# Optimization experiments

Measured on AMD Instinct MI355X. Metric: run time of the kernel, lower is better.

Reference implementation:

```python
import jax, jax.numpy as jnp
import numpy as np

B, S, D = 32, 512, 512      # batch, seq, feature
E, H, O, K = 8, 2048, 512, 2  # experts, expert hidden, expert out, top_k


def setup_inputs() -> dict:
    key = jax.random.key(0)
    ks = jax.random.split(key, 5)
    sc = lambda k, shape, scale: jax.random.normal(k, shape, jnp.float32) * scale
    return {
        "x": sc(ks[0], (B, S, D), 1.0),
        "attn_w": sc(ks[1], (D, 1), 0.05),
        "attn_b": jnp.zeros((1,), jnp.float32),
        "gate_w": sc(ks[2], (D, E), 0.05),
        "gate_b": jnp.zeros((E,), jnp.float32),
        "w1": sc(ks[3], (E, D, H), 0.02),
        "b1": jnp.zeros((E, H), jnp.float32),
        "w2": sc(ks[4], (E, H, O), 0.02),
        "b2": jnp.zeros((E, O), jnp.float32),
    }


def reference(x, attn_w, attn_b, gate_w, gate_b, w1, b1, w2, b2):
    # --- attention pooling over the sequence axis ---
    scores = x @ attn_w + attn_b                      # [B,S,1]
    aw = jax.nn.softmax(scores, axis=1)               # softmax over seq
    pooled = jnp.sum(x * aw, axis=1)                  # [B,D]

    # --- gating: softmax -> top-k mask -> renormalize ---
    gates = jax.nn.softmax(pooled @ gate_w + gate_b, axis=-1)  # [B,E]
    _, idx = jax.lax.top_k(gates, K)                  # [B,K]
    mask = jnp.sum(jax.nn.one_hot(idx, E, dtype=gates.dtype), axis=-2)  # [B,E]
    g = gates * mask
    g = g / (jnp.sum(g, axis=-1, keepdims=True) + 1e-9)        # [B,E]

    # --- dense all-experts compute (exact GELU, as keras Dense('gelu')) ---
    h = jax.nn.gelu(jnp.einsum('bsd,edh->ebsh', x, w1) + b1[:, None, None, :],
                    approximate=False)                 # [E,B,S,H]
    eo = jax.nn.gelu(jnp.einsum('ebsh,eho->ebso', h, w2) + b2[:, None, None, :],
                     approximate=False)                # [E,B,S,O]

    # --- weighted combine over experts ---
    return jnp.einsum('ebso,be->bso', eo, g)           # [B,S,O]
```

## Files before the change

kernel.cpp:

```cpp
#include <hip/hip_runtime.h>
#include <hip/hip_bf16.h>
#include <math.h>

#define B_  32
#define S_  512
#define D_  512
#define E_  8
#define H_  2048
#define O_  512

typedef __bf16 bf16x8 __attribute__((ext_vector_type(8)));
typedef float  f32x4  __attribute__((ext_vector_type(4)));

#define GL2LDS(src, dst) \
  __builtin_amdgcn_global_load_lds((const __attribute__((address_space(1))) void*)(src), \
                                   (__attribute__((address_space(3))) void*)(dst), 16, 0, 0)

__device__ __forceinline__ float gelu_exact(float v) {
  return 0.5f * v * (1.0f + erff(v * 0.70710678118654752f));
}

__global__ __launch_bounds__(256) void pool_gate_kernel(
    const float* __restrict__ x, const float* __restrict__ attn_w,
    const float* __restrict__ attn_b, const float* __restrict__ gate_w,
    const float* __restrict__ gate_b, int* __restrict__ gidx, float* __restrict__ gwt)
{
  __shared__ float sc[512];
  __shared__ float pooled[512];
  __shared__ float red[8];
  const int tid = threadIdx.x;
  const int b = blockIdx.x;
  const float* xb = x + (size_t)b * S_ * D_;
  const float ab = attn_b[0];

  for (int s = tid; s < S_; s += 256) {
    const float4* xr = (const float4*)(xb + (size_t)s * D_);
    const float4* wr = (const float4*)attn_w;
    float acc = 0.f;
    for (int i = 0; i < D_ / 4; ++i) {
      float4 xv = xr[i], wv = wr[i];
      acc += xv.x * wv.x + xv.y * wv.y + xv.z * wv.z + xv.w * wv.w;
    }
    sc[s] = acc + ab;
  }
  __syncthreads();

  float m = fmaxf(sc[tid], sc[tid + 256]);
  for (int off = 32; off; off >>= 1) m = fmaxf(m, __shfl_down(m, off));
  if ((tid & 63) == 0) red[tid >> 6] = m;
  __syncthreads();
  if (tid == 0) red[0] = fmaxf(fmaxf(red[0], red[1]), fmaxf(red[2], red[3]));
  __syncthreads();
  m = red[0];
  float e0 = expf(sc[tid] - m), e1 = expf(sc[tid + 256] - m);
  float ssum = e0 + e1;
  for (int off = 32; off; off >>= 1) ssum += __shfl_down(ssum, off);
  if ((tid & 63) == 0) red[4 + (tid >> 6)] = ssum;
  __syncthreads();
  if (tid == 0) red[4] = red[4] + red[5] + red[6] + red[7];
  __syncthreads();
  float inv = 1.f / red[4];
  sc[tid] = e0 * inv;
  sc[tid + 256] = e1 * inv;
  __syncthreads();

  float p0 = 0.f, p1 = 0.f;
  for (int s = 0; s < S_; ++s) {
    float awv = sc[s];
    p0 += awv * xb[(size_t)s * D_ + tid];
    p1 += awv * xb[(size_t)s * D_ + tid + 256];
  }
  pooled[tid] = p0;
  pooled[tid + 256] = p1;
  __syncthreads();

  if (tid < E_) {
    float z = gate_b[tid];
    for (int d = 0; d < D_; ++d) z += pooled[d] * gate_w[d * E_ + tid];
    red[tid] = z;
  }
  __syncthreads();
  if (tid == 0) {
    float zmax = red[0];
    for (int i = 1; i < E_; ++i) zmax = fmaxf(zmax, red[i]);
    float ge[E_]; float zs = 0.f;
    for (int i = 0; i < E_; ++i) { ge[i] = expf(red[i] - zmax); zs += ge[i]; }
    for (int i = 0; i < E_; ++i) ge[i] /= zs;
    int i0 = 0;
    for (int i = 1; i < E_; ++i) if (ge[i] > ge[i0]) i0 = i;
    int i1 = -1;
    for (int i = 0; i < E_; ++i) if (i != i0 && (i1 < 0 || ge[i] > ge[i1])) i1 = i;
    float denom = ge[i0] + ge[i1] + 1e-9f;
    gidx[b * 2 + 0] = i0; gidx[b * 2 + 1] = i1;
    gwt[b * 2 + 0] = ge[i0] / denom; gwt[b * 2 + 1] = ge[i1] / denom;
  }
}

__global__ void cast_x_kernel(const float* __restrict__ in, ushort* __restrict__ outp, int n) {
  int i = blockIdx.x * blockDim.x + threadIdx.x;
  const int n4 = n >> 2;
  for (; i < n4; i += gridDim.x * blockDim.x) {
    float4 v = ((const float4*)in)[i];
    ushort4 o;
    o.x = __builtin_bit_cast(unsigned short, __float2bfloat16(v.x));
    o.y = __builtin_bit_cast(unsigned short, __float2bfloat16(v.y));
    o.z = __builtin_bit_cast(unsigned short, __float2bfloat16(v.z));
    o.w = __builtin_bit_cast(unsigned short, __float2bfloat16(v.w));
    ((ushort4*)outp)[i] = o;
  }
}

__global__ void transpose_cast_kernel(const float* __restrict__ in,
                                      __hip_bfloat16* __restrict__ outT, int R, int C)
{
  __shared__ float tile[32][33];
  const int z = blockIdx.z;
  const float* inz = in + (size_t)z * R * C;
  __hip_bfloat16* outz = outT + (size_t)z * R * C;
  const int c0 = blockIdx.x * 32, r0 = blockIdx.y * 32;
  const int tx = threadIdx.x, ty = threadIdx.y;
#pragma unroll
  for (int jj = 0; jj < 4; ++jj) {
    int r = r0 + ty + jj * 8;
    tile[ty + jj * 8][tx] = inz[(size_t)r * C + c0 + tx];
  }
  __syncthreads();
#pragma unroll
  for (int jj = 0; jj < 4; ++jj) {
    int c = c0 + ty + jj * 8;
    outz[(size_t)c * R + r0 + tx] = __float2bfloat16(tile[tx][ty + jj * 8]);
  }
}

__device__ __forceinline__ void stage_tile(char* lds, const __hip_bfloat16* g, int ldk, int kt, int tid) {
#pragma unroll
  for (int i = 0; i < 4; ++i) {
    int f = (i * 256 + tid) * 16;
    int row = f >> 7;
    int colb = (f & 127) ^ ((row & 7) << 4);
    const char* src = (const char*)g + ((size_t)row * ldk + kt) * 2 + colb;
    GL2LDS(src, lds + f);
  }
}

__device__ __forceinline__ void gemm_tiles(const __hip_bfloat16* Ag, const __hip_bfloat16* Bg,
                                           int K, char* As, char* Bs, f32x4 (&acc)[4][4])
{
  const int tid = threadIdx.x;
  const int l = tid & 63;
  const int w = tid >> 6;
  const int wm = (w >> 1) << 6;
  const int wn = (w & 1) << 6;
  const int lr = l & 15;
  const int kg = (l >> 4) << 3;
  for (int kt = 0; kt < K; kt += 64) {
    __syncthreads();
    stage_tile(As, Ag, K, kt, tid);
    stage_tile(Bs, Bg, K, kt, tid);
    __syncthreads();
#pragma unroll
    for (int kk = 0; kk < 2; ++kk) {
      const int kb = (kk * 32 + kg) * 2;
      bf16x8 af[4], bfv[4];
#pragma unroll
      for (int i = 0; i < 4; ++i) {
        int ra = wm + i * 16 + lr;
        af[i] = *(const bf16x8*)(As + ra * 128 + (kb ^ ((ra & 7) << 4)));
        int rb = wn + i * 16 + lr;
        bfv[i] = *(const bf16x8*)(Bs + rb * 128 + (kb ^ ((rb & 7) << 4)));
      }
#pragma unroll
      for (int mi = 0; mi < 4; ++mi)
#pragma unroll
        for (int ni = 0; ni < 4; ++ni)
          acc[mi][ni] = __builtin_amdgcn_mfma_f32_16x16x32_bf16(af[mi], bfv[ni], acc[mi][ni], 0, 0, 0);
    }
  }
}

__global__ __launch_bounds__(256, 2) void gemm1_kernel(
    const __hip_bfloat16* __restrict__ Xb, const __hip_bfloat16* __restrict__ W1T,
    const float* __restrict__ b1, __hip_bfloat16* __restrict__ Hbuf,
    const int* __restrict__ gidx, int p0)
{
  __shared__ char lds[32768];
  char* As = lds; char* Bs = lds + 16384;
  const int p = p0 + blockIdx.y;
  const int b = p >> 1;
  const int e = gidx[p];
  const int s0 = (blockIdx.x >> 4) * 128;
  const int h0 = (blockIdx.x & 15) * 128;
  const __hip_bfloat16* Ag = Xb + ((size_t)b * S_ + s0) * D_;
  const __hip_bfloat16* Bg = W1T + ((size_t)e * H_ + h0) * D_;
  f32x4 acc[4][4] = {};
  gemm_tiles(Ag, Bg, D_, As, Bs, acc);

  const int tid = threadIdx.x, l = tid & 63, w = tid >> 6;
  const int wm = (w >> 1) << 6, wn = (w & 1) << 6;
  const int r4 = (l >> 4) << 2, cc = l & 15;
  const float* b1e = b1 + (size_t)e * H_ + h0;
  __hip_bfloat16* Hb = Hbuf + ((size_t)blockIdx.y * S_ + s0) * H_ + h0;
#pragma unroll
  for (int mi = 0; mi < 4; ++mi) {
    int row = wm + mi * 16 + r4;
#pragma unroll
    for (int ni = 0; ni < 4; ++ni) {
      int col = wn + ni * 16 + cc;
      float bias = b1e[col];
      __hip_bfloat16* dst = Hb + (size_t)row * H_ + col;
#pragma unroll
      for (int j = 0; j < 4; ++j) {
        float v = gelu_exact(acc[mi][ni][j] + bias);
        dst[(size_t)j * H_] = __float2bfloat16(v);
      }
    }
  }
}

__global__ __launch_bounds__(256, 2) void gemm2_kernel(
    const __hip_bfloat16* __restrict__ Hbuf, const __hip_bfloat16* __restrict__ W2T,
    const float* __restrict__ b2, float* __restrict__ out,
    const int* __restrict__ gidx, const float* __restrict__ gwt, int p0)
{
  __shared__ char lds[32768];
  char* As = lds; char* Bs = lds + 16384;
  const int p = p0 + blockIdx.y;
  const int b = p >> 1;
  const int e = gidx[p];
  const float gw = gwt[p];
  const int s0 = (blockIdx.x >> 2) * 128;
  const int o0 = (blockIdx.x & 3) * 128;
  const __hip_bfloat16* Ag = Hbuf + ((size_t)blockIdx.y * S_ + s0) * H_;
  const __hip_bfloat16* Bg = W2T + ((size_t)e * O_ + o0) * H_;
  f32x4 acc[4][4] = {};
  gemm_tiles(Ag, Bg, H_, As, Bs, acc);

  const int tid = threadIdx.x, l = tid & 63, w = tid >> 6;
  const int wm = (w >> 1) << 6, wn = (w & 1) << 6;
  const int r4 = (l >> 4) << 2, cc = l & 15;
  const float* b2e = b2 + (size_t)e * O_ + o0;
  float* ob = out + ((size_t)b * S_ + s0) * O_ + o0;
#pragma unroll
  for (int mi = 0; mi < 4; ++mi) {
    int row = wm + mi * 16 + r4;
#pragma unroll
    for (int ni = 0; ni < 4; ++ni) {
      int col = wn + ni * 16 + cc;
      float bias = b2e[col];
      float* dst = ob + (size_t)row * O_ + col;
#pragma unroll
      for (int j = 0; j < 4; ++j) {
        float v = gelu_exact(acc[mi][ni][j] + bias) * gw;
        atomicAdd(dst + (size_t)j * O_, v);
      }
    }
  }
}

__global__ void sentinel_kernel(float* out, int n) {
  int i = blockIdx.x * blockDim.x + threadIdx.x;
  for (; i < n; i += gridDim.x * blockDim.x) out[i] = 1.0e6f;
}

extern "C" void kernel_launch(void* const* d_in, const int* in_sizes, int n_in,
                              void* d_out, int out_size, void* d_ws, size_t ws_size,
                              hipStream_t stream)
{
  const float* x      = (const float*)d_in[0];
  const float* attn_w = (const float*)d_in[1];
  const float* attn_b = (const float*)d_in[2];
  const float* gate_w = (const float*)d_in[3];
  const float* gate_b = (const float*)d_in[4];
  const float* w1     = (const float*)d_in[5];
  const float* b1     = (const float*)d_in[6];
  const float* w2     = (const float*)d_in[7];
  const float* b2     = (const float*)d_in[8];
  float* out = (float*)d_out;

  char* ws = (char*)d_ws;
  const size_t OFF_GIDX = 0;
  const size_t OFF_GWT  = 256;
  const size_t OFF_X    = 512;
  const size_t SZ_X     = (size_t)B_ * S_ * D_ * 2;
  const size_t OFF_W1T  = OFF_X + SZ_X;
  const size_t SZ_W1T   = (size_t)E_ * H_ * D_ * 2;
  const size_t OFF_W2T  = OFF_W1T + SZ_W1T;
  const size_t SZ_W2T   = (size_t)E_ * O_ * H_ * 2;
  const size_t OFF_H    = OFF_W2T + SZ_W2T;
  const size_t PAIR_H   = (size_t)S_ * H_ * 2;

  int G = 64;
  while (G > 1 && OFF_H + (size_t)G * PAIR_H > ws_size) G >>= 1;
  if (OFF_H + (size_t)G * PAIR_H > ws_size) {
    hipLaunchKernelGGL(sentinel_kernel, dim3(256), dim3(256), 0, stream, out, out_size);
    return;
  }

  int*   gidx = (int*)(ws + OFF_GIDX);
  float* gwt  = (float*)(ws + OFF_GWT);
  __hip_bfloat16* xb   = (__hip_bfloat16*)(ws + OFF_X);
  __hip_bfloat16* w1T  = (__hip_bfloat16*)(ws + OFF_W1T);
  __hip_bfloat16* w2T  = (__hip_bfloat16*)(ws + OFF_W2T);
  __hip_bfloat16* Hbuf = (__hip_bfloat16*)(ws + OFF_H);

  hipLaunchKernelGGL(pool_gate_kernel, dim3(B_), dim3(256), 0, stream,
                     x, attn_w, attn_b, gate_w, gate_b, gidx, gwt);
  hipLaunchKernelGGL(cast_x_kernel, dim3(2048), dim3(256), 0, stream,
                     x, (ushort*)xb, B_ * S_ * D_);
  hipLaunchKernelGGL(transpose_cast_kernel, dim3(H_ / 32, D_ / 32, E_), dim3(32, 8), 0, stream,
                     w1, w1T, D_, H_);
  hipLaunchKernelGGL(transpose_cast_kernel, dim3(O_ / 32, H_ / 32, E_), dim3(32, 8), 0, stream,
                     w2, w2T, H_, O_);
  hipMemsetAsync(d_out, 0, (size_t)out_size * sizeof(float), stream);

  for (int p0 = 0; p0 < B_ * 2; p0 += G) {
    hipLaunchKernelGGL(gemm1_kernel, dim3(64, G), dim3(256), 0, stream,
                       xb, w1T, b1, Hbuf, gidx, p0);
    hipLaunchKernelGGL(gemm2_kernel, dim3(16, G), dim3(256), 0, stream,
                       Hbuf, w2T, b2, out, gidx, gwt, p0);
  }
}
```

Measured before the change: 310.0 us.

## Use 256x256 double-buffered GEMM tiles with 512 threads and staged prefetch

Replaces the 128x128 single-buffered GEMM core with a 256x256 tile over 8 waves that double-buffers K-slices in 128KB of dynamic LDS. The loads for the next slice are split into four chunks and issued between MFMA phases, so global-to-LDS traffic overlaps compute. Operands are swapped so weights feed the A side, and epilogues use vectorized bias loads and stores. It also drops the group loop and launches all 64 pairs in one grid each. The larger tiles raise register and LDS pressure, which could limit occupancy, and the requested 2 blocks per CU would need 256KB of LDS, which may not fit.

After: 485.0 us. +56.5%, slower.

```diff
diff --git a/kernel.cpp b/kernel.cpp
--- a/kernel.cpp
+++ b/kernel.cpp
@@ -132,127 +132,198 @@
   }
 }
 
-__device__ __forceinline__ void stage_tile(char* lds, const __hip_bfloat16* g, int ldk, int kt, int tid) {
-#pragma unroll
-  for (int i = 0; i < 4; ++i) {
-    int f = (i * 256 + tid) * 16;
-    int row = f >> 7;
-    int colb = (f & 127) ^ ((row & 7) << 4);
-    const char* src = (const char*)g + ((size_t)row * ldk + kt) * 2 + colb;
-    GL2LDS(src, lds + f);
-  }
-}
-
-__device__ __forceinline__ void gemm_tiles(const __hip_bfloat16* Ag, const __hip_bfloat16* Bg,
-                                           int K, char* As, char* Bs, f32x4 (&acc)[4][4])
+__device__ __forceinline__ void gemm256(const char* __restrict__ Ag, const char* __restrict__ Bg,
+                                        const int ldb, const int NT, char* lds, f32x4 (&acc)[8][4])
 {
   const int tid = threadIdx.x;
   const int l = tid & 63;
   const int w = tid >> 6;
-  const int wm = (w >> 1) << 6;
-  const int wn = (w & 1) << 6;
+  const int wr = w >> 2;
+  const int wc = w & 3;
   const int lr = l & 15;
-  const int kg = (l >> 4) << 3;
-  for (int kt = 0; kt < K; kt += 64) {
-    __syncthreads();
-    stage_tile(As, Ag, K, kt, tid);
-    stage_tile(Bs, Bg, K, kt, tid);
-    __syncthreads();
-#pragma unroll
-    for (int kk = 0; kk < 2; ++kk) {
-      const int kb = (kk * 32 + kg) * 2;
-      bf16x8 af[4], bfv[4];
-#pragma unroll
-      for (int i = 0; i < 4; ++i) {
-        int ra = wm + i * 16 + lr;
-        af[i] = *(const bf16x8*)(As + ra * 128 + (kb ^ ((ra & 7) << 4)));
-        int rb = wn + i * 16 + lr;
-        bfv[i] = *(const bf16x8*)(Bs + rb * 128 + (kb ^ ((rb & 7) << 4)));
-      }
-#pragma unroll
-      for (int mi = 0; mi < 4; ++mi)
-#pragma unroll
-        for (int ni = 0; ni < 4; ++ni)
-          acc[mi][ni] = __builtin_amdgcn_mfma_f32_16x16x32_bf16(af[mi], bfv[ni], acc[mi][ni], 0, 0, 0);
-    }
-  }
-}
-
-__global__ __launch_bounds__(256, 2) void gemm1_kernel(
+  const int hi16 = ((l >> 4) & 3) << 4;
+  const int axor = (lr & 7) << 4;
+  const int k0 = (0   + hi16) ^ axor;
+  const int k1 = (64  + hi16) ^ axor;
+  const int abase = wr * 16384 + lr * 128;
+  const int bbase = 32768 + wc * 8192 + lr * 128;
+
+  const int rw = tid >> 3;
+  const int cs = ((tid & 7) << 4) ^ ((rw & 7) << 4);
+  const char* sA00 = Ag + (size_t)(  0 +  0 + rw) * ldb + cs;
+  const char* sA01 = Ag + (size_t)(  0 + 64 + rw) * ldb + cs;
+  const char* sA10 = Ag + (size_t)(128 +  0 + rw) * ldb + cs;
+  const char* sA11 = Ag + (size_t)(128 + 64 + rw) * ldb + cs;
+  const char* sB00 = Bg + (size_t)(  0 +  0 + rw) * ldb + cs;
+  const char* sB01 = Bg + (size_t)(  0 + 64 + rw) * ldb + cs;
+  const char* sB10 = Bg + (size_t)(128 +  0 + rw) * ldb + cs;
+  const char* sB11 = Bg + (size_t)(128 + 64 + rw) * ldb + cs;
+  const int dst = tid * 16;
+
+  GL2LDS(sA00, lds + dst);            GL2LDS(sA01, lds +  8192 + dst);
+  GL2LDS(sA10, lds + 16384 + dst);    GL2LDS(sA11, lds + 24576 + dst);
+  GL2LDS(sB00, lds + 32768 + dst);    GL2LDS(sB01, lds + 40960 + dst);
+  GL2LDS(sB10, lds + 49152 + dst);    GL2LDS(sB11, lds + 57344 + dst);
+  sA00 += 128; sA01 += 128; sA10 += 128; sA11 += 128;
+  sB00 += 128; sB01 += 128; sB10 += 128; sB11 += 128;
+
+  for (int t = 0; t < NT; ++t) {
+    char* cur = lds + ((t & 1) << 16);
+    char* nxt = lds + (((t + 1) & 1) << 16);
+    const bool pre = (t + 1 < NT);
+    bf16x8 bf[4][2];
+    bf16x8 af[2][2];
+
+    if (pre) { GL2LDS(sA00, nxt + dst); GL2LDS(sA01, nxt + 8192 + dst); }
+    if (pre) asm volatile("s_waitcnt vmcnt(2)" ::: "memory");
+    else     asm volatile("s_waitcnt vmcnt(0)" ::: "memory");
+    __builtin_amdgcn_s_barrier();
+    __builtin_amdgcn_sched_barrier(0);
+#pragma unroll
+    for (int n = 0; n < 4; ++n) {
+      bf[n][0] = *(const bf16x8*)(cur + bbase + n * 2048 + k0);
+      bf[n][1] = *(const bf16x8*)(cur + bbase + n * 2048 + k1);
+    }
+    af[0][0] = *(const bf16x8*)(cur + abase + 0 * 2048 + k0);
+    af[0][1] = *(const bf16x8*)(cur + abase + 0 * 2048 + k1);
+    af[1][0] = *(const bf16x8*)(cur + abase + 1 * 2048 + k0);
+    af[1][1] = *(const bf16x8*)(cur + abase + 1 * 2048 + k1);
+    __builtin_amdgcn_s_setprio(1);
+#pragma unroll
+    for (int rr = 0; rr < 2; ++rr)
+#pragma unroll
+      for (int n = 0; n < 4; ++n)
+#pragma unroll
+        for (int kh = 0; kh < 2; ++kh)
+          acc[0 + rr][n] = __builtin_amdgcn_mfma_f32_16x16x32_bf16(af[rr][kh], bf[n][kh], acc[0 + rr][n], 0, 0, 0);
+    __builtin_amdgcn_s_setprio(0);
+    __builtin_amdgcn_s_barrier();
+
+    if (pre) { GL2LDS(sA10, nxt + 16384 + dst); GL2LDS(sA11, nxt + 24576 + dst); }
+    af[0][0] = *(const bf16x8*)(cur + abase + 2 * 2048 + k0);
+    af[0][1] = *(const bf16x8*)(cur + abase + 2 * 2048 + k1);
+    af[1][0] = *(const bf16x8*)(cur + abase + 3 * 2048 + k0);
+    af[1][1] = *(const bf16x8*)(cur + abase + 3 * 2048 + k1);
+    __builtin_amdgcn_s_setprio(1);
+#pragma unroll
+    for (int rr = 0; rr < 2; ++rr)
+#pragma unroll
+      for (int n = 0; n < 4; ++n)
+#pragma unroll
+        for (int kh = 0; kh < 2; ++kh)
+          acc[2 + rr][n] = __builtin_amdgcn_mfma_f32_16x16x32_bf16(af[rr][kh], bf[n][kh], acc[2 + rr][n], 0, 0, 0);
+    __builtin_amdgcn_s_setprio(0);
+    __builtin_amdgcn_s_barrier();
+
+    if (pre) { GL2LDS(sB00, nxt + 32768 + dst); GL2LDS(sB01, nxt + 40960 + dst); }
+    af[0][0] = *(const bf16x8*)(cur + abase + 4 * 2048 + k0);
+    af[0][1] = *(const bf16x8*)(cur + abase + 4 * 2048 + k1);
+    af[1][0] = *(const bf16x8*)(cur + abase + 5 * 2048 + k0);
+    af[1][1] = *(const bf16x8*)(cur + abase + 5 * 2048 + k1);
+    __builtin_amdgcn_s_setprio(1);
+#pragma unroll
+    for (int rr = 0; rr < 2; ++rr)
+#pragma unroll
+      for (int n = 0; n < 4; ++n)
+#pragma unroll
+        for (int kh = 0; kh < 2; ++kh)
+          acc[4 + rr][n] = __builtin_amdgcn_mfma_f32_16x16x32_bf16(af[rr][kh], bf[n][kh], acc[4 + rr][n], 0, 0, 0);
+    __builtin_amdgcn_s_setprio(0);
+    __builtin_amdgcn_s_barrier();
+
+    if (pre) { GL2LDS(sB10, nxt + 49152 + dst); GL2LDS(sB11, nxt + 57344 + dst); }
+    af[0][0] = *(const bf16x8*)(cur + abase + 6 * 2048 + k0);
+    af[0][1] = *(const bf16x8*)(cur + abase + 6 * 2048 + k1);
+    af[1][0] = *(const bf16x8*)(cur + abase + 7 * 2048 + k0);
+    af[1][1] = *(const bf16x8*)(cur + abase + 7 * 2048 + k1);
+    __builtin_amdgcn_s_setprio(1);
+#pragma unroll
+    for (int rr = 0; rr < 2; ++rr)
+#pragma unroll
+      for (int n = 0; n < 4; ++n)
+#pragma unroll
+        for (int kh = 0; kh < 2; ++kh)
+          acc[6 + rr][n] = __builtin_amdgcn_mfma_f32_16x16x32_bf16(af[rr][kh], bf[n][kh], acc[6 + rr][n], 0, 0, 0);
+    __builtin_amdgcn_s_setprio(0);
+    __builtin_amdgcn_sched_barrier(0);
+    __builtin_amdgcn_s_barrier();
+
+    if (pre) {
+      sA00 += 128; sA01 += 128; sA10 += 128; sA11 += 128;
+      sB00 += 128; sB01 += 128; sB10 += 128; sB11 += 128;
+    }
+  }
+}
+
+__global__ __launch_bounds__(512, 2) void gemm1_kernel(
     const __hip_bfloat16* __restrict__ Xb, const __hip_bfloat16* __restrict__ W1T,
     const float* __restrict__ b1, __hip_bfloat16* __restrict__ Hbuf,
-    const int* __restrict__ gidx, int p0)
-{
-  __shared__ char lds[32768];
-  char* As = lds; char* Bs = lds + 16384;
-  const int p = p0 + blockIdx.y;
+    const int* __restrict__ gidx)
+{
+  extern __shared__ char lds[];
+  const int p = blockIdx.y;
   const int b = p >> 1;
   const int e = gidx[p];
-  const int s0 = (blockIdx.x >> 4) * 128;
-  const int h0 = (blockIdx.x & 15) * 128;
-  const __hip_bfloat16* Ag = Xb + ((size_t)b * S_ + s0) * D_;
-  const __hip_bfloat16* Bg = W1T + ((size_t)e * H_ + h0) * D_;
-  f32x4 acc[4][4] = {};
-  gemm_tiles(Ag, Bg, D_, As, Bs, acc);
+  const int sc0 = (blockIdx.x >> 3) * 256;
+  const int h0  = (blockIdx.x & 7) * 256;
+  const char* Ag = (const char*)(W1T + ((size_t)e * H_ + h0) * D_);
+  const char* Bg = (const char*)(Xb + ((size_t)b * S_ + sc0) * D_);
+  f32x4 acc[8][4] = {};
+  gemm256(Ag, Bg, D_ * 2, D_ / 64, lds, acc);
 
   const int tid = threadIdx.x, l = tid & 63, w = tid >> 6;
-  const int wm = (w >> 1) << 6, wn = (w & 1) << 6;
-  const int r4 = (l >> 4) << 2, cc = l & 15;
+  const int wr = w >> 2, wc = w & 3, lr = l & 15, hi4 = ((l >> 4) & 3) << 2;
   const float* b1e = b1 + (size_t)e * H_ + h0;
-  __hip_bfloat16* Hb = Hbuf + ((size_t)blockIdx.y * S_ + s0) * H_ + h0;
-#pragma unroll
-  for (int mi = 0; mi < 4; ++mi) {
-    int row = wm + mi * 16 + r4;
-#pragma unroll
-    for (int ni = 0; ni < 4; ++ni) {
-      int col = wn + ni * 16 + cc;
-      float bias = b1e[col];
-      __hip_bfloat16* dst = Hb + (size_t)row * H_ + col;
-#pragma unroll
-      for (int j = 0; j < 4; ++j) {
-        float v = gelu_exact(acc[mi][ni][j] + bias);
-        dst[(size_t)j * H_] = __float2bfloat16(v);
-      }
-    }
-  }
-}
-
-__global__ __launch_bounds__(256, 2) void gemm2_kernel(
+  __hip_bfloat16* Hp = Hbuf + (size_t)p * S_ * H_;
+#pragma unroll
+  for (int r = 0; r < 8; ++r) {
+    const int hl = wr * 128 + r * 16 + hi4;
+    const float4 bias = *(const float4*)(b1e + hl);
+#pragma unroll
+    for (int n = 0; n < 4; ++n) {
+      const int sl = sc0 + wc * 64 + n * 16 + lr;
+      ushort4 ov;
+      ov.x = __builtin_bit_cast(unsigned short, __float2bfloat16(gelu_exact(acc[r][n][0] + bias.x)));
+      ov.y = __builtin_bit_cast(unsigned short, __float2bfloat16(gelu_exact(acc[r][n][1] + bias.y)));
+      ov.z = __builtin_bit_cast(unsigned short, __float2bfloat16(gelu_exact(acc[r][n][2] + bias.z)));
+      ov.w = __builtin_bit_cast(unsigned short, __float2bfloat16(gelu_exact(acc[r][n][3] + bias.w)));
+      *(ushort4*)(Hp + (size_t)sl * H_ + h0 + hl) = ov;
+    }
+  }
+}
+
+__global__ __launch_bounds__(512, 2) void gemm2_kernel(
     const __hip_bfloat16* __restrict__ Hbuf, const __hip_bfloat16* __restrict__ W2T,
     const float* __restrict__ b2, float* __restrict__ out,
-    const int* __restrict__ gidx, const float* __restrict__ gwt, int p0)
-{
-  __shared__ char lds[32768];
-  char* As = lds; char* Bs = lds + 16384;
-  const int p = p0 + blockIdx.y;
+    const int* __restrict__ gidx, const float* __restrict__ gwt)
+{
+  extern __shared__ char lds[];
+  const int p = blockIdx.y;
   const int b = p >> 1;
   const int e = gidx[p];
   const float gw = gwt[p];
-  const int s0 = (blockIdx.x >> 2) * 128;
-  const int o0 = (blockIdx.x & 3) * 128;
-  const __hip_bfloat16* Ag = Hbuf + ((size_t)blockIdx.y * S_ + s0) * H_;
-  const __hip_bfloat16* Bg = W2T + ((size_t)e * O_ + o0) * H_;
-  f32x4 acc[4][4] = {};
-  gemm_tiles(Ag, Bg, H_, As, Bs, acc);
+  const int sc0 = (blockIdx.x >> 1) * 256;
+  const int o0  = (blockIdx.x & 1) * 256;
+  const char* Ag = (const char*)(W2T + ((size_t)e * O_ + o0) * H_);
+  const char* Bg = (const char*)(Hbuf + ((size_t)p * S_ + sc0) * H_);
+  f32x4 acc[8][4] = {};
+  gemm256(Ag, Bg, H_ * 2, H_ / 64, lds, acc);
 
   const int tid = threadIdx.x, l = tid & 63, w = tid >> 6;
-  const int wm = (w >> 1) << 6, wn = (w & 1) << 6;
-  const int r4 = (l >> 4) << 2, cc = l & 15;
+  const int wr = w >> 2, wc = w & 3, lr = l & 15, hi4 = ((l >> 4) & 3) << 2;
   const float* b2e = b2 + (size_t)e * O_ + o0;
-  float* ob = out + ((size_t)b * S_ + s0) * O_ + o0;
-#pragma unroll
-  for (int mi = 0; mi < 4; ++mi) {
-    int row = wm + mi * 16 + r4;
-#pragma unroll
-    for (int ni = 0; ni < 4; ++ni) {
-      int col = wn + ni * 16 + cc;
-      float bias = b2e[col];
-      float* dst = ob + (size_t)row * O_ + col;
-#pragma unroll
-      for (int j = 0; j < 4; ++j) {
-        float v = gelu_exact(acc[mi][ni][j] + bias) * gw;
-        atomicAdd(dst + (size_t)j * O_, v);
-      }
+#pragma unroll
+  for (int r = 0; r < 8; ++r) {
+    const int ol = wr * 128 + r * 16 + hi4;
+    const float4 bias = *(const float4*)(b2e + ol);
+#pragma unroll
+    for (int n = 0; n < 4; ++n) {
+      const int sl = sc0 + wc * 64 + n * 16 + lr;
+      float* dst = out + ((size_t)b * S_ + sl) * O_ + o0 + ol;
+      atomicAdd(dst + 0, gelu_exact(acc[r][n][0] + bias.x) * gw);
+      atomicAdd(dst + 1, gelu_exact(acc[r][n][1] + bias.y) * gw);
+      atomicAdd(dst + 2, gelu_exact(acc[r][n][2] + bias.z) * gw);
+      atomicAdd(dst + 3, gelu_exact(acc[r][n][3] + bias.w) * gw);
     }
   }
 }
@@ -289,9 +360,7 @@
   const size_t OFF_H    = OFF_W2T + SZ_W2T;
   const size_t PAIR_H   = (size_t)S_ * H_ * 2;
 
-  int G = 64;
-  while (G > 1 && OFF_H + (size_t)G * PAIR_H > ws_size) G >>= 1;
-  if (OFF_H + (size_t)G * PAIR_H > ws_size) {
+  if (OFF_H + 64 * PAIR_H > ws_size) {
     hipLaunchKernelGGL(sentinel_kernel, dim3(256), dim3(256), 0, stream, out, out_size);
     return;
   }
@@ -302,6 +371,9 @@
   __hip_bfloat16* w1T  = (__hip_bfloat16*)(ws + OFF_W1T);
   __hip_bfloat16* w2T  = (__hip_bfloat16*)(ws + OFF_W2T);
   __hip_bfloat16* Hbuf = (__hip_bfloat16*)(ws + OFF_H);
+
+  (void)hipFuncSetAttribute((const void*)gemm1_kernel, hipFuncAttributeMaxDynamicSharedMemorySize, 131072);
+  (void)hipFuncSetAttribute((const void*)gemm2_kernel, hipFuncAttributeMaxDynamicSharedMemorySize, 131072);
 
   hipLaunchKernelGGL(pool_gate_kernel, dim3(B_), dim3(256), 0, stream,
                      x, attn_w, attn_b, gate_w, gate_b, gidx, gwt);
@@ -313,10 +385,8 @@
                      w2, w2T, H_, O_);
   hipMemsetAsync(d_out, 0, (size_t)out_size * sizeof(float), stream);
 
-  for (int p0 = 0; p0 < B_ * 2; p0 += G) {
-    hipLaunchKernelGGL(gemm1_kernel, dim3(64, G), dim3(256), 0, stream,
-                       xb, w1T, b1, Hbuf, gidx, p0);
-    hipLaunchKernelGGL(gemm2_kernel, dim3(16, G), dim3(256), 0, stream,
-                       Hbuf, w2T, b2, out, gidx, gwt, p0);
-  }
-}
+  hipLaunchKernelGGL(gemm1_kernel, dim3(16, 64), dim3(512), 131072, stream,
+                     xb, w1T, b1, Hbuf, gidx);
+  hipLaunchKernelGGL(gemm2_kernel, dim3(4, 64), dim3(512), 131072, stream,
+                     Hbuf, w2T, b2, out, gidx, gwt);
+}
```

## Use 128x256 triple-buffered MFMA GEMM tiles with expert-sorted, XCD-aware block mapping

Applied to the files above, without the earlier changes.

Replaces the 128x128, 4-wave, single-buffered GEMM loop with a 128x256, 8-wave kernel. It uses a three-stage LDS ring fed by direct global-to-LDS loads, explicit vmcnt waits, raw barriers and s_setprio around the MFMA bursts, so the next tiles load while the current one is computed. A new single-thread kernel sorts token/expert pairs by expert, and blocks are remapped across XCDs so blocks sharing an expert's weights are co-scheduled for L2 reuse. The pair-group loop is collapsed into one launch per GEMM, which now requires the full H buffer in workspace. The 144KB of dynamic LDS limits occupancy to one block per CU.

Result: slower. 342.5 us (+10.5%).

```diff
diff --git a/kernel.cpp b/kernel.cpp
--- a/kernel.cpp
+++ b/kernel.cpp
@@ -96,6 +96,17 @@
   }
 }
 
+__global__ void psort_kernel(const int* __restrict__ gidx, int* __restrict__ psort) {
+  if (threadIdx.x == 0 && blockIdx.x == 0) {
+    int cnt[E_];
+    for (int e = 0; e < E_; ++e) cnt[e] = 0;
+    for (int p = 0; p < 2 * B_; ++p) cnt[gidx[p]]++;
+    int pos[E_]; int s = 0;
+    for (int e = 0; e < E_; ++e) { pos[e] = s; s += cnt[e]; }
+    for (int p = 0; p < 2 * B_; ++p) psort[pos[gidx[p]]++] = p;
+  }
+}
+
 __global__ void cast_x_kernel(const float* __restrict__ in, ushort* __restrict__ outp, int n) {
   int i = blockIdx.x * blockDim.x + threadIdx.x;
   const int n4 = n >> 2;
@@ -132,126 +143,178 @@
   }
 }
 
-__device__ __forceinline__ void stage_tile(char* lds, const __hip_bfloat16* g, int ldk, int kt, int tid) {
-#pragma unroll
-  for (int i = 0; i < 4; ++i) {
-    int f = (i * 256 + tid) * 16;
-    int row = f >> 7;
-    int colb = (f & 127) ^ ((row & 7) << 4);
-    const char* src = (const char*)g + ((size_t)row * ldk + kt) * 2 + colb;
-    GL2LDS(src, lds + f);
-  }
-}
-
-__device__ __forceinline__ void gemm_tiles(const __hip_bfloat16* Ag, const __hip_bfloat16* Bg,
-                                           int K, char* As, char* Bs, f32x4 (&acc)[4][4])
+__device__ __forceinline__ void gemm128x256(const char* __restrict__ Ag, const char* __restrict__ Bg,
+                                            const int lda, const int ldbb, const int NT,
+                                            char* lds, f32x4 (&acc)[4][4])
 {
   const int tid = threadIdx.x;
   const int l = tid & 63;
   const int w = tid >> 6;
-  const int wm = (w >> 1) << 6;
-  const int wn = (w & 1) << 6;
+  const int wr = w >> 2;
+  const int wc = w & 3;
   const int lr = l & 15;
-  const int kg = (l >> 4) << 3;
-  for (int kt = 0; kt < K; kt += 64) {
-    __syncthreads();
-    stage_tile(As, Ag, K, kt, tid);
-    stage_tile(Bs, Bg, K, kt, tid);
-    __syncthreads();
-#pragma unroll
-    for (int kk = 0; kk < 2; ++kk) {
-      const int kb = (kk * 32 + kg) * 2;
+  const int kc16 = ((l >> 4) & 3) << 4;
+  const int swz = (lr & 7) << 4;
+  const int kA = kc16 ^ swz;
+  const int kB = (64 + kc16) ^ swz;
+  const int aoff = (wr * 64 + lr) * 128;
+  const int boff = 16384 + (wc * 64 + lr) * 128;
+
+  const int rw = tid >> 3;
+  const int cs = ((tid & 7) << 4) ^ ((rw & 7) << 4);
+  const int dst = tid * 16;
+  const char* pA0 = Ag + (size_t)(rw      ) * lda  + cs;
+  const char* pA1 = Ag + (size_t)(rw +  64) * lda  + cs;
+  const char* pB0 = Bg + (size_t)(rw      ) * ldbb + cs;
+  const char* pB1 = Bg + (size_t)(rw +  64) * ldbb + cs;
+  const char* pB2 = Bg + (size_t)(rw + 128) * ldbb + cs;
+  const char* pB3 = Bg + (size_t)(rw + 192) * ldbb + cs;
+
+  {
+    char* q0 = lds;
+    GL2LDS(pA0, q0 + dst);          GL2LDS(pA1, q0 + 8192 + dst);
+    GL2LDS(pB0, q0 + 16384 + dst);  GL2LDS(pB1, q0 + 24576 + dst);
+    GL2LDS(pB2, q0 + 32768 + dst);  GL2LDS(pB3, q0 + 40960 + dst);
+    char* q1 = lds + 49152;
+    GL2LDS(pA0 + 128, q1 + dst);          GL2LDS(pA1 + 128, q1 + 8192 + dst);
+    GL2LDS(pB0 + 128, q1 + 16384 + dst);  GL2LDS(pB1 + 128, q1 + 24576 + dst);
+    GL2LDS(pB2 + 128, q1 + 32768 + dst);  GL2LDS(pB3 + 128, q1 + 40960 + dst);
+    pA0 += 256; pA1 += 256; pB0 += 256; pB1 += 256; pB2 += 256; pB3 += 256;
+  }
+
+  for (int t = 0; t < NT; ++t) {
+    char* cur = lds + (t % 3) * 49152;
+    char* nb  = lds + ((t + 2) % 3) * 49152;
+    const bool pre = (t + 2 < NT);
+
+    if (pre) {
+      GL2LDS(pA0, nb + dst);
+      GL2LDS(pA1, nb + 8192 + dst);
+      GL2LDS(pB0, nb + 16384 + dst);
+    }
+    if (pre)             asm volatile("s_waitcnt vmcnt(9)" ::: "memory");
+    else if (t + 1 < NT) asm volatile("s_waitcnt vmcnt(6)" ::: "memory");
+    else                 asm volatile("s_waitcnt vmcnt(0)" ::: "memory");
+    __builtin_amdgcn_s_barrier();
+    __builtin_amdgcn_sched_barrier(0);
+    {
       bf16x8 af[4], bfv[4];
 #pragma unroll
-      for (int i = 0; i < 4; ++i) {
-        int ra = wm + i * 16 + lr;
-        af[i] = *(const bf16x8*)(As + ra * 128 + (kb ^ ((ra & 7) << 4)));
-        int rb = wn + i * 16 + lr;
-        bfv[i] = *(const bf16x8*)(Bs + rb * 128 + (kb ^ ((rb & 7) << 4)));
-      }
-#pragma unroll
-      for (int mi = 0; mi < 4; ++mi)
-#pragma unroll
-        for (int ni = 0; ni < 4; ++ni)
-          acc[mi][ni] = __builtin_amdgcn_mfma_f32_16x16x32_bf16(af[mi], bfv[ni], acc[mi][ni], 0, 0, 0);
-    }
-  }
-}
-
-__global__ __launch_bounds__(256, 2) void gemm1_kernel(
+      for (int r = 0; r < 4; ++r) af[r]  = *(const bf16x8*)(cur + aoff + r * 2048 + kA);
+#pragma unroll
+      for (int n = 0; n < 4; ++n) bfv[n] = *(const bf16x8*)(cur + boff + n * 2048 + kA);
+      __builtin_amdgcn_s_setprio(1);
+#pragma unroll
+      for (int r = 0; r < 4; ++r)
+#pragma unroll
+        for (int n = 0; n < 4; ++n)
+          acc[r][n] = __builtin_amdgcn_mfma_f32_16x16x32_bf16(af[r], bfv[n], acc[r][n], 0, 0, 0);
+      __builtin_amdgcn_s_setprio(0);
+    }
+    __builtin_amdgcn_sched_barrier(0);
+    __builtin_amdgcn_s_barrier();
+
+    if (pre) {
+      GL2LDS(pB1, nb + 24576 + dst);
+      GL2LDS(pB2, nb + 32768 + dst);
+      GL2LDS(pB3, nb + 40960 + dst);
+      pA0 += 128; pA1 += 128; pB0 += 128; pB1 += 128; pB2 += 128; pB3 += 128;
+    }
+    {
+      bf16x8 af[4], bfv[4];
+#pragma unroll
+      for (int r = 0; r < 4; ++r) af[r]  = *(const bf16x8*)(cur + aoff + r * 2048 + kB);
+#pragma unroll
+      for (int n = 0; n < 4; ++n) bfv[n] = *(const bf16x8*)(cur + boff + n * 2048 + kB);
+      __builtin_amdgcn_s_setprio(1);
+#pragma unroll
+      for (int r = 0; r < 4; ++r)
+#pragma unroll
+        for (int n = 0; n < 4; ++n)
+          acc[r][n] = __builtin_amdgcn_mfma_f32_16x16x32_bf16(af[r], bfv[n], acc[r][n], 0, 0, 0);
+      __builtin_amdgcn_s_setprio(0);
+    }
+    __builtin_amdgcn_sched_barrier(0);
+    __builtin_amdgcn_s_barrier();
+  }
+}
+
+__global__ __launch_bounds__(512, 2) void gemm1_kernel(
     const __hip_bfloat16* __restrict__ Xb, const __hip_bfloat16* __restrict__ W1T,
     const float* __restrict__ b1, __hip_bfloat16* __restrict__ Hbuf,
-    const int* __restrict__ gidx, int p0)
-{
-  __shared__ char lds[32768];
-  char* As = lds; char* Bs = lds + 16384;
-  const int p = p0 + blockIdx.y;
+    const int* __restrict__ gidx, const int* __restrict__ psort)
+{
+  extern __shared__ char lds[];
+  const int nblk = gridDim.x * gridDim.y;
+  const int P = blockIdx.y * gridDim.x + blockIdx.x;
+  const int L = (P & 7) * (nblk >> 3) + (P >> 3);
+  const int pairL = L >> 5;
+  const int tl = L & 31;
+  const int p = psort[pairL];
   const int b = p >> 1;
   const int e = gidx[p];
-  const int s0 = (blockIdx.x >> 4) * 128;
-  const int h0 = (blockIdx.x & 15) * 128;
-  const __hip_bfloat16* Ag = Xb + ((size_t)b * S_ + s0) * D_;
-  const __hip_bfloat16* Bg = W1T + ((size_t)e * H_ + h0) * D_;
+  const int s0 = (tl >> 3) * 128;
+  const int h0 = (tl & 7) * 256;
+  const char* Ag = (const char*)(Xb + ((size_t)b * S_ + s0) * D_);
+  const char* Bg = (const char*)(W1T + ((size_t)e * H_ + h0) * D_);
   f32x4 acc[4][4] = {};
-  gemm_tiles(Ag, Bg, D_, As, Bs, acc);
+  gemm128x256(Ag, Bg, D_ * 2, D_ * 2, D_ / 64, lds, acc);
 
   const int tid = threadIdx.x, l = tid & 63, w = tid >> 6;
-  const int wm = (w >> 1) << 6, wn = (w & 1) << 6;
-  const int r4 = (l >> 4) << 2, cc = l & 15;
+  const int wr = w >> 2, wc = w & 3, lr = l & 15, kc4 = ((l >> 4) & 3) << 2;
   const float* b1e = b1 + (size_t)e * H_ + h0;
-  __hip_bfloat16* Hb = Hbuf + ((size_t)blockIdx.y * S_ + s0) * H_ + h0;
-#pragma unroll
-  for (int mi = 0; mi < 4; ++mi) {
-    int row = wm + mi * 16 + r4;
-#pragma unroll
-    for (int ni = 0; ni < 4; ++ni) {
-      int col = wn + ni * 16 + cc;
-      float bias = b1e[col];
-      __hip_bfloat16* dst = Hb + (size_t)row * H_ + col;
+  __hip_bfloat16* Hp = Hbuf + (size_t)p * S_ * H_ + h0;
+#pragma unroll
+  for (int r = 0; r < 4; ++r) {
+#pragma unroll
+    for (int n = 0; n < 4; ++n) {
+      const int hl = wc * 64 + n * 16 + lr;
+      const float bias = b1e[hl];
 #pragma unroll
       for (int j = 0; j < 4; ++j) {
-        float v = gelu_exact(acc[mi][ni][j] + bias);
-        dst[(size_t)j * H_] = __float2bfloat16(v);
+        const int s = s0 + wr * 64 + r * 16 + kc4 + j;
+        Hp[(size_t)s * H_ + hl] = __float2bfloat16(gelu_exact(acc[r][n][j] + bias));
       }
     }
   }
 }
 
-__global__ __launch_bounds__(256, 2) void gemm2_kernel(
+__global__ __launch_bounds__(512, 2) void gemm2_kernel(
     const __hip_bfloat16* __restrict__ Hbuf, const __hip_bfloat16* __restrict__ W2T,
     const float* __restrict__ b2, float* __restrict__ out,
-    const int* __restrict__ gidx, const float* __restrict__ gwt, int p0)
-{
-  __shared__ char lds[32768];
-  char* As = lds; char* Bs = lds + 16384;
-  const int p = p0 + blockIdx.y;
+    const int* __restrict__ gidx, const float* __restrict__ gwt, const int* __restrict__ psort)
+{
+  extern __shared__ char lds[];
+  const int nblk = gridDim.x * gridDim.y;
+  const int P = blockIdx.y * gridDim.x + blockIdx.x;
+  const int L = (P & 7) * (nblk >> 3) + (P >> 3);
+  const int pairL = L >> 3;
+  const int tl = L & 7;
+  const int p = psort[pairL];
   const int b = p >> 1;
   const int e = gidx[p];
   const float gw = gwt[p];
-  const int s0 = (blockIdx.x >> 2) * 128;
-  const int o0 = (blockIdx.x & 3) * 128;
-  const __hip_bfloat16* Ag = Hbuf + ((size_t)blockIdx.y * S_ + s0) * H_;
-  const __hip_bfloat16* Bg = W2T + ((size_t)e * O_ + o0) * H_;
+  const int s0 = (tl >> 1) * 128;
+  const int o0 = (tl & 1) * 256;
+  const char* Ag = (const char*)(Hbuf + ((size_t)p * S_ + s0) * H_);
+  const char* Bg = (const char*)(W2T + ((size_t)e * O_ + o0) * H_);
   f32x4 acc[4][4] = {};
-  gemm_tiles(Ag, Bg, H_, As, Bs, acc);
+  gemm128x256(Ag, Bg, H_ * 2, H_ * 2, H_ / 64, lds, acc);
 
   const int tid = threadIdx.x, l = tid & 63, w = tid >> 6;
-  const int wm = (w >> 1) << 6, wn = (w & 1) << 6;
-  const int r4 = (l >> 4) << 2, cc = l & 15;
+  const int wr = w >> 2, wc = w & 3, lr = l & 15, kc4 = ((l >> 4) & 3) << 2;
   const float* b2e = b2 + (size_t)e * O_ + o0;
-  float* ob = out + ((size_t)b * S_ + s0) * O_ + o0;
-#pragma unroll
-  for (int mi = 0; mi < 4; ++mi) {
-    int row = wm + mi * 16 + r4;
-#pragma unroll
-    for (int ni = 0; ni < 4; ++ni) {
-      int col = wn + ni * 16 + cc;
-      float bias = b2e[col];
-      float* dst = ob + (size_t)row * O_ + col;
+#pragma unroll
+  for (int r = 0; r < 4; ++r) {
+#pragma unroll
+    for (int n = 0; n < 4; ++n) {
+      const int ol = wc * 64 + n * 16 + lr;
+      const float bias = b2e[ol];
 #pragma unroll
       for (int j = 0; j < 4; ++j) {
-        float v = gelu_exact(acc[mi][ni][j] + bias) * gw;
-        atomicAdd(dst + (size_t)j * O_, v);
+        const int s = s0 + wr * 64 + r * 16 + kc4 + j;
+        atomicAdd(out + ((size_t)b * S_ + s) * O_ + o0 + ol,
+                  gelu_exact(acc[r][n][j] + bias) * gw);
       }
     }
   }
@@ -280,7 +343,8 @@
   char* ws = (char*)d_ws;
   const size_t OFF_GIDX = 0;
   const size_t OFF_GWT  = 256;
-  const size_t OFF_X    = 512;
+  const size_t OFF_PSRT = 512;
+  const size_t OFF_X    = 1024;
   const size_t SZ_X     = (size_t)B_ * S_ * D_ * 2;
   const size_t OFF_W1T  = OFF_X + SZ_X;
   const size_t SZ_W1T   = (size_t)E_ * H_ * D_ * 2;
@@ -289,22 +353,25 @@
   const size_t OFF_H    = OFF_W2T + SZ_W2T;
   const size_t PAIR_H   = (size_t)S_ * H_ * 2;
 
-  int G = 64;
-  while (G > 1 && OFF_H + (size_t)G * PAIR_H > ws_size) G >>= 1;
-  if (OFF_H + (size_t)G * PAIR_H > ws_size) {
+  if (OFF_H + 64 * PAIR_H > ws_size) {
     hipLaunchKernelGGL(sentinel_kernel, dim3(256), dim3(256), 0, stream, out, out_size);
     return;
   }
 
-  int*   gidx = (int*)(ws + OFF_GIDX);
-  float* gwt  = (float*)(ws + OFF_GWT);
+  int*   gidx  = (int*)(ws + OFF_GIDX);
+  float* gwt   = (float*)(ws + OFF_GWT);
+  int*   psort = (int*)(ws + OFF_PSRT);
   __hip_bfloat16* xb   = (__hip_bfloat16*)(ws + OFF_X);
   __hip_bfloat16* w1T  = (__hip_bfloat16*)(ws + OFF_W1T);
   __hip_bfloat16* w2T  = (__hip_bfloat16*)(ws + OFF_W2T);
   __hip_bfloat16* Hbuf = (__hip_bfloat16*)(ws + OFF_H);
 
+  (void)hipFuncSetAttribute((const void*)gemm1_kernel, hipFuncAttributeMaxDynamicSharedMemorySize, 147456);
+  (void)hipFuncSetAttribute((const void*)gemm2_kernel, hipFuncAttributeMaxDynamicSharedMemorySize, 147456);
+
   hipLaunchKernelGGL(pool_gate_kernel, dim3(B_), dim3(256), 0, stream,
                      x, attn_w, attn_b, gate_w, gate_b, gidx, gwt);
+  hipLaunchKernelGGL(psort_kernel, dim3(1), dim3(64), 0, stream, gidx, psort);
   hipLaunchKernelGGL(cast_x_kernel, dim3(2048), dim3(256), 0, stream,
                      x, (ushort*)xb, B_ * S_ * D_);
   hipLaunchKernelGGL(transpose_cast_kernel, dim3(H_ / 32, D_ / 32, E_), dim3(32, 8), 0, stream,
@@ -313,10 +380,8 @@
                      w2, w2T, H_, O_);
   hipMemsetAsync(d_out, 0, (size_t)out_size * sizeof(float), stream);
 
-  for (int p0 = 0; p0 < B_ * 2; p0 += G) {
-    hipLaunchKernelGGL(gemm1_kernel, dim3(64, G), dim3(256), 0, stream,
-                       xb, w1T, b1, Hbuf, gidx, p0);
-    hipLaunchKernelGGL(gemm2_kernel, dim3(16, G), dim3(256), 0, stream,
-                       Hbuf, w2T, b2, out, gidx, gwt, p0);
-  }
-}
+  hipLaunchKernelGGL(gemm1_kernel, dim3(32, 64), dim3(512), 147456, stream,
+                     xb, w1T, b1, Hbuf, gidx, psort);
+  hipLaunchKernelGGL(gemm2_kernel, dim3(8, 64), dim3(512), 147456, stream,
+                     Hbuf, w2T, b2, out, gidx, gwt, psort);
+}
```
